# Optimization experiments

Hardware: AMD Instinct MI355X
Metric: run time of the kernel (lower is better)

The kernel has to match this reference:

```python
import jax, jax.numpy as jnp
import numpy as np

D_MODEL = 256      # num_nodes == d_model (forced by pre_relation mask shape)
MW = 2             # moving_window (hardcoded '2' in MPNN reshape)
STRIDE = 1
DECAY = 0.7
INPUT_DIM = 64
OUTPUT_DIM = 64
BN_EPS = 1e-5


def _mask_matrix():
    # Mask_Matrix: block (i,j) of size d_model x d_model equals decay**|i-j|
    blocks = DECAY ** np.abs(np.arange(MW)[:, None] - np.arange(MW)[None, :])
    return jnp.asarray(np.kron(blocks, np.ones((D_MODEL, D_MODEL))).astype(np.float32))


def _bn(h, w, b):
    # training-mode BatchNorm1d over channel-last layout [B, N, C]
    mu = h.mean(axis=(0, 1))
    var = h.var(axis=(0, 1))  # biased variance, as torch uses for normalization
    return (h - mu) * jax.lax.rsqrt(var + BN_EPS) * w + b


def setup_inputs() -> dict:
    key = jax.random.key(0)
    ks = jax.random.split(key, 4)
    bs, scale_num = 16, 17
    x = jax.random.normal(ks[0], (bs, scale_num, D_MODEL, INPUT_DIM), jnp.float32)
    # mapping2 weights scaled small to keep the dot-product softmax well conditioned
    w_map2 = jax.random.normal(ks[1], (INPUT_DIM, INPUT_DIM), jnp.float32) * 0.05
    b_map2 = jnp.zeros((INPUT_DIM,), jnp.float32)
    bn0_w = jnp.ones((INPUT_DIM,), jnp.float32)
    bn0_b = jnp.zeros((INPUT_DIM,), jnp.float32)
    th0_w = jax.random.normal(ks[2], (OUTPUT_DIM, INPUT_DIM), jnp.float32) / np.float32(np.sqrt(INPUT_DIM))
    th0_b = jnp.zeros((OUTPUT_DIM,), jnp.float32)
    th1_w = jax.random.normal(ks[3], (OUTPUT_DIM, INPUT_DIM), jnp.float32) / np.float32(np.sqrt(INPUT_DIM))
    th1_b = jnp.zeros((OUTPUT_DIM,), jnp.float32)
    bn1_w = jnp.ones((OUTPUT_DIM,), jnp.float32)
    bn1_b = jnp.zeros((OUTPUT_DIM,), jnp.float32)
    return dict(x=x, w_map2=w_map2, b_map2=b_map2, bn0_w=bn0_w, bn0_b=bn0_b,
                th0_w=th0_w, th0_b=th0_b, th1_w=th1_w, th1_b=th1_b,
                bn1_w=bn1_w, bn1_b=bn1_b)


def reference(x, w_map2, b_map2, bn0_w, bn0_b, th0_w, th0_b, th1_w, th1_b, bn1_w, bn1_b):
    bs, S, N, F = x.shape
    L = (S - MW) // STRIDE + 1  # num_windows from F.unfold
    # WindowConv_Graph + transpose(2,3) + reshape: X[b,l,m,n,f] = x[b, l*stride+m, n, f]
    idx = np.arange(L)[:, None] * STRIDE + np.arange(MW)[None, :]
    X = x[:, idx].reshape(bs * L, MW * N, F)  # [B', N1, F]

    # Dot_Graph_Construction_weights (N1 != d_model -> mapping2 branch)
    nf = X @ w_map2.T + b_map2                       # [B', N1, F]
    adj = jnp.einsum('bnf,bmf->bnm', nf, nf)         # [B', N1, N1]
    eye = jnp.eye(MW * N, dtype=x.dtype)
    adj = jax.nn.leaky_relu(adj - eye * 1e8)
    adj = jax.nn.softmax(adj, axis=-1) + eye

    # decay mask multiply
    adj = adj * _mask_matrix()

    # BatchNorm over input_dim channels
    xb = _bn(nf, bn0_w, bn0_b)

    # MPNN_mk_v2, field=2, way='sum'
    out = (adj @ xb) @ th0_w.T + th0_b               # hop 1
    adj2 = adj @ adj
    out = out + (adj2 @ xb) @ th1_w.T + th1_b        # hop 2
    out = jax.nn.leaky_relu(_bn(out, bn1_w, bn1_b))

    # pooling over the moving_window axis (mean), then over windows (mean)
    out = out.reshape(bs, L, MW, N, OUTPUT_DIM).mean(axis=2)
    return out.mean(axis=1)  # [bs, num_nodes, output_dim]
```

## Files before the change

kernel.cpp:

```cpp
#include <hip/hip_runtime.h>


typedef unsigned short u16;
typedef __bf16 bf16x8 __attribute__((ext_vector_type(8)));
typedef float f32x4 __attribute__((ext_vector_type(4)));
typedef unsigned int u32x4 __attribute__((ext_vector_type(4)));

#define MFMA16(a, b, c) __builtin_amdgcn_mfma_f32_16x16x32_bf16(a, b, c, 0, 0, 0)

#define BSZ 16
#define SNUM 17
#define FD 64
#define NB 256
#define N1 512
#define SL_ELEMS 16384
#define Y_ELEMS (BSZ * SNUM * SL_ELEMS)

#define WM_O 0
#define BM_O 4096
#define B0W_O 4160
#define B0B_O 4224
#define T0W_O 4288
#define T0B_O 8384
#define T1W_O 8448
#define T1B_O 12544
#define B1W_O 12608
#define B1B_O 12672
#define P_TOT 12736

#define SLAB2_O 32768
#define RED_O 65536
#define SCR_O 65792
#define LDS_BYTES ((SCR_O + 16 * 640) * 2)

__device__ __forceinline__ float bf2f(u16 u) {
    union { unsigned int i; float f; } v;
    v.i = ((unsigned int)u) << 16;
    return v.f;
}
__device__ __forceinline__ u16 f2bu(float f) {
    __bf16 h = (__bf16)f;
    return __builtin_bit_cast(u16, h);
}
__device__ __forceinline__ u16 f2bf(float f) {
    unsigned int u = __builtin_bit_cast(unsigned int, f);
    unsigned int r = (u + 0x7fffu + ((u >> 16) & 1u)) >> 16;
    return (u16)r;
}
__device__ __forceinline__ bf16x8 ld8g(const u16* p) {
    return __builtin_bit_cast(bf16x8, *reinterpret_cast<const u32x4*>(p));
}

__global__ __launch_bounds__(256) void k_prep(
    const void* p0, const void* p1, const void* p2, const void* p3,
    const void* p4, const void* p5, const void* p6, const void* p7,
    const void* p8, const void* p9, int* __restrict__ flagOut,
    u16* __restrict__ pc, float* __restrict__ stats) {
    const int tid = threadIdx.x, lane = tid & 63;
    int z = 0, bc = 0;
    const unsigned int* w = (const unsigned int*)p0;
    for (int i = lane; i < 2048; i += 64) {
        const unsigned int v = w[i];
        z += ((v & 0xffffu) == 0u);
        bc += (v >> 14) & 1;
    }
#pragma unroll
    for (int o = 1; o < 64; o <<= 1) {
        z += __shfl_xor(z, o);
        bc += __shfl_xor(bc, o);
    }
    const int flag = (z > 1024 || bc > 256) ? 1 : 0;
    if (blockIdx.x == 0) {
        if (tid == 0) *flagOut = flag;
        if (tid < 256) stats[tid] = 0.f;
    }
    const int i = blockIdx.x * 256 + tid;
    if (i >= P_TOT) return;
    const void* src;
    int si;
    if (i < BM_O)        { src = p0; si = i; }
    else if (i < B0W_O)  { src = p1; si = i - BM_O; }
    else if (i < B0B_O)  { src = p2; si = i - B0W_O; }
    else if (i < T0W_O)  { src = p3; si = i - B0B_O; }
    else if (i < T0B_O)  { src = p4; si = i - T0W_O; }
    else if (i < T1W_O)  { src = p5; si = i - T0B_O; }
    else if (i < T1B_O)  { src = p6; si = i - T1W_O; }
    else if (i < B1W_O)  { src = p7; si = i - T1B_O; }
    else if (i < B1B_O)  { src = p8; si = i - B1W_O; }
    else                 { src = p9; si = i - B1B_O; }
    pc[i] = flag ? f2bf(((const float*)src)[si]) : ((const u16*)src)[si];
}

__global__ __launch_bounds__(256) void k_y(const void* __restrict__ xv,
                                           const int* __restrict__ flag,
                                           const u16* __restrict__ pc,
                                           u16* __restrict__ y,
                                           float* __restrict__ gstats) {
    const int slice = blockIdx.x;
    const int tid = threadIdx.x, wave = tid >> 6, lane = tid & 63;
    const int quad = lane >> 4, l16 = lane & 15;
    __shared__ float red[128];
    if (tid < 128) red[tid] = 0.f;
    const int isf32 = *flag;

    f32x4 acc[4][4];
#pragma unroll
    for (int i = 0; i < 4; i++)
#pragma unroll
        for (int j = 0; j < 4; j++) acc[i][j] = (f32x4){0.f, 0.f, 0.f, 0.f};

    bf16x8 bfr[4][2];
#pragma unroll
    for (int nt = 0; nt < 4; nt++)
#pragma unroll
        for (int kh = 0; kh < 2; kh++)
            bfr[nt][kh] = ld8g(pc + WM_O + (nt * 16 + l16) * 64 + kh * 32 + quad * 8);

    const float* xf = (const float*)xv + (size_t)slice * SL_ELEMS;
    const u16* xh = (const u16*)xv + (size_t)slice * SL_ELEMS;

#pragma unroll
    for (int mt = 0; mt < 4; mt++) {
        const int row = wave * 64 + mt * 16 + l16;
        bf16x8 a0, a1;
        if (isf32) {
            const float* r0 = xf + row * 64 + quad * 8;
            f32x4 v0 = *(const f32x4*)r0;
            f32x4 v1 = *(const f32x4*)(r0 + 4);
            f32x4 v2 = *(const f32x4*)(r0 + 32);
            f32x4 v3 = *(const f32x4*)(r0 + 36);
#pragma unroll
            for (int j = 0; j < 4; j++) {
                a0[j] = (__bf16)v0[j]; a0[4 + j] = (__bf16)v1[j];
                a1[j] = (__bf16)v2[j]; a1[4 + j] = (__bf16)v3[j];
            }
        } else {
            a0 = ld8g(xh + row * 64 + quad * 8);
            a1 = ld8g(xh + row * 64 + 32 + quad * 8);
        }
#pragma unroll
        for (int nt = 0; nt < 4; nt++)
            acc[mt][nt] = MFMA16(a1, bfr[nt][1], MFMA16(a0, bfr[nt][0], acc[mt][nt]));
    }

    u16* ys = y + (size_t)slice * SL_ELEMS;
    float s1[4] = {0.f, 0.f, 0.f, 0.f}, s2[4] = {0.f, 0.f, 0.f, 0.f};
#pragma unroll
    for (int nt = 0; nt < 4; nt++) {
        const int col = nt * 16 + l16;
        const float bias = bf2f(pc[BM_O + col]);
#pragma unroll
        for (int mt = 0; mt < 4; mt++)
#pragma unroll
            for (int r = 0; r < 4; r++) {
                const int row = wave * 64 + mt * 16 + quad * 4 + r;
                const float v = acc[mt][nt][r] + bias;
                ys[row * 64 + col] = f2bu(v);
                s1[nt] += v;
                s2[nt] += v * v;
            }
        s1[nt] += __shfl_xor(s1[nt], 16); s1[nt] += __shfl_xor(s1[nt], 32);
        s2[nt] += __shfl_xor(s2[nt], 16); s2[nt] += __shfl_xor(s2[nt], 32);
    }
    __syncthreads();
    if (quad == 0) {
#pragma unroll
        for (int nt = 0; nt < 4; nt++) {
            atomicAdd(&red[nt * 16 + l16], s1[nt]);
            atomicAdd(&red[64 + nt * 16 + l16], s2[nt]);
        }
    }
    __syncthreads();
    const int s = slice % SNUM;
    const float wgt = (s == 0 || s == SNUM - 1) ? 1.f : 2.f;
    if (tid < 128) atomicAdd(&gstats[tid], red[tid] * wgt);
}

__global__ __launch_bounds__(1024)
__attribute__((amdgpu_waves_per_eu(4, 4)))
void k_mega(
    const u16* __restrict__ y, float* __restrict__ stats,
    const u16* __restrict__ pc, u16* __restrict__ opre) {
    extern __shared__ u16 lds[];
    u16* slab1 = lds;
    u16* slab2 = lds + SLAB2_O;
    float* red = (float*)(lds + RED_O);
    const int tid = threadIdx.x, w = tid >> 6, lane = tid & 63;
    const int quad = lane >> 4, l16 = lane & 15;
    u16* scr = lds + SCR_O + w * 640;
    const int p = blockIdx.x, b = p >> 4, l = p & 15;
    const f32x4 ZERO4 = (f32x4){0.f, 0.f, 0.f, 0.f};

    if (tid < 128) red[tid] = 0.f;

    const float cinv = 1.f / 131072.f;
    const int fme = tid & 63;
    float mu0 = stats[fme] * cinv;
    float vr0 = fmaxf(stats[64 + fme] * cinv - mu0 * mu0, 0.f);
    const float scale_f = rsqrtf(vr0 + 1e-5f) * bf2f(pc[B0W_O + fme]);
    const float shift_f = bf2f(pc[B0B_O + fme]) - mu0 * scale_f;

    const u16* ybase = y + (size_t)(b * SNUM + l) * SL_ELEMS;
#pragma unroll
    for (int i = 0; i < 4; i++) {
        const int gid = i * 1024 + tid, n = gid >> 3, g = gid & 7;
        *(u32x4*)(slab1 + n * 64 + ((g ^ (n & 7)) << 3)) =
            *(const u32x4*)(ybase + n * 64 + g * 8);
    }
    __syncthreads();

#pragma unroll
    for (int i = 0; i < 4; i++) {
        const int gn = (tid >> 6) + i * 16;
        union { u16 u[8]; u32x4 v; } pk;
#pragma unroll
        for (int j = 0; j < 8; j++) {
            const int n = gn * 8 + j;
            const u16 raw = slab1[n * 64 + (((fme >> 3) ^ (n & 7)) << 3) + (fme & 7)];
            pk.u[j] = f2bu(bf2f(raw) * scale_f + shift_f);
        }
        *(u32x4*)(slab2 + fme * 512 + ((gn ^ fme) << 3)) = pk.v;
    }
    __syncthreads();

    bf16x8 a[2][2];
#pragma unroll
    for (int st = 0; st < 2; st++)
#pragma unroll
        for (int h = 0; h < 2; h++) {
            const int row = w * 32 + st * 16 + l16;
            a[st][h] = *(const bf16x8*)(slab1 + row * 64 + (((h * 4 + quad) ^ (row & 7)) << 3));
        }

    for (int pass = 0; pass < 2; pass++) {
        f32x4 oacc[2][4];
        f32x4 lsum[2];
#pragma unroll
        for (int st = 0; st < 2; st++) {
            lsum[st] = ZERO4;
#pragma unroll
            for (int ft = 0; ft < 4; ft++) oacc[st][ft] = ZERO4;
        }

        for (int c = 0; c < 8; c++) {
            const float mf = ((w >= 8) == (c >= 4)) ? 1.f : 0.7f;
#pragma unroll
            for (int ch = 0; ch < 2; ch++) {
                const int colbase = c * 64 + ch * 32;
                f32x4 S[2][2];
#pragma unroll
                for (int jt = 0; jt < 2; jt++) {
                    const int rj = colbase + jt * 16 + l16;
                    const bf16x8 b0 = *(const bf16x8*)(slab1 + rj * 64 + ((quad ^ (rj & 7)) << 3));
                    const bf16x8 b1 = *(const bf16x8*)(slab1 + rj * 64 + (((4 + quad) ^ (rj & 7)) << 3));
#pragma unroll
                    for (int st = 0; st < 2; st++)
                        S[st][jt] = MFMA16(a[st][1], b1, MFMA16(a[st][0], b0, ZERO4));
                }
                bf16x8 pa[2];
#pragma unroll
                for (int st = 0; st < 2; st++) {
                    const int rowbase = w * 32 + st * 16;
#pragma unroll
                    for (int jt = 0; jt < 2; jt++)
#pragma unroll
                        for (int r = 0; r < 4; r++) {
                            const float s = S[st][jt][r];
                            const float m2 = s > 0.f ? 1.44269504f : 0.0144269504f;
                            float pv = exp2f(fminf(s * m2, 86.f));
                            if (colbase + jt * 16 == rowbase && l16 == quad * 4 + r) pv = 0.f;
                            lsum[st][r] += pv;
                            scr[(quad * 4 + r) * 40 + jt * 16 + l16] = f2bu(pv * mf);
                        }
                    pa[st] = *(const bf16x8*)(scr + l16 * 40 + quad * 8);
                }
#pragma unroll
                for (int ft = 0; ft < 4; ft++) {
                    const int f = ft * 16 + l16, gn = c * 8 + ch * 4 + quad;
                    const bf16x8 bv = *(const bf16x8*)(slab2 + f * 512 + ((gn ^ f) << 3));
                    oacc[0][ft] = MFMA16(pa[0], bv, oacc[0][ft]);
                    oacc[1][ft] = MFMA16(pa[1], bv, oacc[1][ft]);
                }
            }
        }
#pragma unroll
        for (int st = 0; st < 2; st++)
#pragma unroll
            for (int r = 0; r < 4; r++) {
                lsum[st][r] += __shfl_xor(lsum[st][r], 1);
                lsum[st][r] += __shfl_xor(lsum[st][r], 2);
                lsum[st][r] += __shfl_xor(lsum[st][r], 4);
                lsum[st][r] += __shfl_xor(lsum[st][r], 8);
            }

        if (pass == 0) {
#pragma unroll
            for (int st = 0; st < 2; st++) {
                f32x4 inv;
#pragma unroll
                for (int r = 0; r < 4; r++) inv[r] = __builtin_amdgcn_rcpf(lsum[st][r]);
#pragma unroll
                for (int ft = 0; ft < 4; ft++)
#pragma unroll
                    for (int r = 0; r < 4; r++) {
                        const int i = w * 32 + st * 16 + quad * 4 + r;
                        const int f = ft * 16 + l16;
                        const float xbv = bf2f(slab2[f * 512 + (((i >> 3) ^ f) << 3) + (i & 7)]);
                        oacc[st][ft][r] = oacc[st][ft][r] * inv[r] + xbv;
                    }
            }
            __syncthreads();
#pragma unroll
            for (int st = 0; st < 2; st++)
#pragma unroll
                for (int ft = 0; ft < 4; ft++)
#pragma unroll
                    for (int r = 0; r < 4; r++) {
                        const int i = w * 32 + st * 16 + quad * 4 + r;
                        const int f = ft * 16 + l16;
                        slab2[f * 512 + (((i >> 3) ^ f) << 3) + (i & 7)] = f2bu(oacc[st][ft][r]);
                    }
            __syncthreads();
        } else {
            float s1a[4] = {0.f, 0.f, 0.f, 0.f}, s2a[4] = {0.f, 0.f, 0.f, 0.f};
#pragma unroll
            for (int st = 0; st < 2; st++) {
                f32x4 inv;
#pragma unroll
                for (int r = 0; r < 4; r++) inv[r] = __builtin_amdgcn_rcpf(lsum[st][r]);
#pragma unroll
                for (int ft = 0; ft < 4; ft++)
#pragma unroll
                    for (int r = 0; r < 4; r++) {
                        const int i = w * 32 + st * 16 + quad * 4 + r;
                        const int f = ft * 16 + l16;
                        const float o1 = bf2f(slab2[f * 512 + (((i >> 3) ^ f) << 3) + (i & 7)]);
                        oacc[st][ft][r] = oacc[st][ft][r] * inv[r] + o1;
                    }
                bf16x8 a1[2], a2[2];
                const int irow = w * 32 + st * 16 + l16;
#pragma unroll
                for (int h = 0; h < 2; h++)
#pragma unroll
                    for (int j = 0; j < 8; j++) {
                        const int f = h * 32 + quad * 8 + j;
                        const u16 raw = slab2[f * 512 + (((irow >> 3) ^ f) << 3) + (irow & 7)];
                        a1[h][j] = __builtin_bit_cast(__bf16, raw);
                    }
#pragma unroll
                for (int h = 0; h < 2; h++) {
#pragma unroll
                    for (int ftl = 0; ftl < 2; ftl++)
#pragma unroll
                        for (int r = 0; r < 4; r++)
                            scr[(quad * 4 + r) * 40 + ftl * 16 + l16] = f2bu(oacc[st][2 * h + ftl][r]);
                    a2[h] = *(const bf16x8*)(scr + l16 * 40 + quad * 8);
                }
                f32x4 pacc[4];
#pragma unroll
                for (int ot = 0; ot < 4; ot++) {
                    const int o = ot * 16 + l16;
                    const float bias = bf2f(pc[T0B_O + o]) + bf2f(pc[T1B_O + o]);
                    pacc[ot] = (f32x4){bias, bias, bias, bias};
                }
#pragma unroll
                for (int h = 0; h < 2; h++)
#pragma unroll
                    for (int ot = 0; ot < 4; ot++) {
                        const int o = ot * 16 + l16;
                        bf16x8 w0f = ld8g(pc + T0W_O + o * 64 + h * 32 + quad * 8);
                        bf16x8 w1f = ld8g(pc + T1W_O + o * 64 + h * 32 + quad * 8);
                        pacc[ot] = MFMA16(a1[h], w0f, pacc[ot]);
                        pacc[ot] = MFMA16(a2[h], w1f, pacc[ot]);
                    }
#pragma unroll
                for (int ot = 0; ot < 4; ot++)
#pragma unroll
                    for (int r = 0; r < 4; r++) {
                        const int i = w * 32 + st * 16 + quad * 4 + r;
                        const int o = ot * 16 + l16;
                        const float v = pacc[ot][r];
                        s1a[ot] += v;
                        s2a[ot] += v * v;
                        opre[(size_t)p * (N1 * FD) + (size_t)i * 64 + o] = f2bu(v);
                    }
            }
#pragma unroll
            for (int ot = 0; ot < 4; ot++) {
                s1a[ot] += __shfl_xor(s1a[ot], 16); s1a[ot] += __shfl_xor(s1a[ot], 32);
                s2a[ot] += __shfl_xor(s2a[ot], 16); s2a[ot] += __shfl_xor(s2a[ot], 32);
            }
            if (quad == 0) {
#pragma unroll
                for (int ot = 0; ot < 4; ot++) {
                    atomicAdd(&red[ot * 16 + l16], s1a[ot]);
                    atomicAdd(&red[64 + ot * 16 + l16], s2a[ot]);
                }
            }
            __syncthreads();
            if (tid < 128) atomicAdd(&stats[128 + tid], red[tid]);
        }
    }
}

__global__ __launch_bounds__(256) void k_final(const u16* __restrict__ op,
                                               const float* __restrict__ stats,
                                               const u16* __restrict__ pc,
                                               float* __restrict__ out) {
    const int o = blockIdx.x * 256 + threadIdx.x;
    const int f = o & 63, n = (o >> 6) & 255, b = o >> 14;
    const float inv = 1.f / 131072.f;
    const float mu = stats[128 + f] * inv;
    const float var = fmaxf(stats[192 + f] * inv - mu * mu, 0.f);
    const float rs = rsqrtf(var + 1e-5f);
    const float scale = rs * bf2f(pc[B1W_O + f]);
    const float shift = bf2f(pc[B1B_O + f]) - mu * scale;
    float acc = 0.f;
    for (int l = 0; l < 16; l++) {
        const size_t pb = (size_t)(b * 16 + l) * N1 * FD;
#pragma unroll
        for (int m = 0; m < 2; m++) {
            float v = bf2f(op[pb + (size_t)(m * 256 + n) * 64 + f]);
            v = v * scale + shift;
            acc += (v > 0.f ? v : 0.01f * v);
        }
    }
    out[o] = acc * (1.f / 32.f);
}

extern "C" void kernel_launch(void* const* d_in, const int* in_sizes, int n_in,
                              void* d_out, int out_size, void* d_ws, size_t ws_size,
                              hipStream_t stream) {
    char* ws = (char*)d_ws;
    size_t off = 0;
    auto alloc = [&](size_t bytes) { void* pp = ws + off; off += (bytes + 255) & ~(size_t)255; return pp; };
    u16* y = (u16*)alloc((size_t)Y_ELEMS * 2);
    u16* opre = (u16*)alloc((size_t)NB * N1 * FD * 2);
    u16* pc = (u16*)alloc(P_TOT * 2);
    float* stats = (float*)alloc(256 * 4);
    int* flag = (int*)alloc(256);
    float* out = (float*)d_out;

    k_prep<<<50, 256, 0, stream>>>(d_in[1], d_in[2], d_in[3], d_in[4], d_in[5],
                                   d_in[6], d_in[7], d_in[8], d_in[9], d_in[10],
                                   flag, pc, stats);
    k_y<<<BSZ * SNUM, 256, 0, stream>>>(d_in[0], flag, pc, y, stats);
    k_mega<<<NB, 1024, LDS_BYTES, stream>>>(y, stats, pc, opre);
    k_final<<<1024, 256, 0, stream>>>(opre, stats, pc, out);
}
```

Baseline: 196.9 us.

## Split projection epilogue into separate kernel and fold decay mask into exponent

```diff
diff --git a/kernel.cpp b/kernel.cpp
--- a/kernel.cpp
+++ b/kernel.cpp
@@ -29,9 +29,8 @@
 #define P_TOT 12736
 
 #define SLAB2_O 32768
-#define RED_O 65536
-#define SCR_O 65792
-#define LDS_BYTES ((SCR_O + 16 * 640) * 2)
+#define SCR_O 65536
+#define LDS_U16 (SCR_O + 16 * 640)
 
 __device__ __forceinline__ float bf2f(u16 u) {
     union { unsigned int i; float f; } v;
@@ -179,19 +178,17 @@
 __global__ __launch_bounds__(1024)
 __attribute__((amdgpu_waves_per_eu(4, 4)))
 void k_mega(
-    const u16* __restrict__ y, float* __restrict__ stats,
-    const u16* __restrict__ pc, u16* __restrict__ opre) {
-    extern __shared__ u16 lds[];
+    const u16* __restrict__ y, const float* __restrict__ stats,
+    const u16* __restrict__ pc, u16* __restrict__ z1g,
+    float* __restrict__ pz1g) {
+    __shared__ u16 lds[LDS_U16];
     u16* slab1 = lds;
     u16* slab2 = lds + SLAB2_O;
-    float* red = (float*)(lds + RED_O);
     const int tid = threadIdx.x, w = tid >> 6, lane = tid & 63;
     const int quad = lane >> 4, l16 = lane & 15;
     u16* scr = lds + SCR_O + w * 640;
     const int p = blockIdx.x, b = p >> 4, l = p & 15;
     const f32x4 ZERO4 = (f32x4){0.f, 0.f, 0.f, 0.f};
-
-    if (tid < 128) red[tid] = 0.f;
 
     const float cinv = 1.f / 131072.f;
     const int fme = tid & 63;
@@ -232,6 +229,9 @@
             a[st][h] = *(const bf16x8*)(slab1 + row * 64 + (((h * 4 + quad) ^ (row & 7)) << 3));
         }
 
+    const float mb = (w < 8) ? 0.7f : (1.0f / 0.7f);
+    const float me = (w < 8) ? (1.0f / 0.7f) : 1.0f;
+
     for (int pass = 0; pass < 2; pass++) {
         f32x4 oacc[2][4];
         f32x4 lsum[2];
@@ -243,7 +243,13 @@
         }
 
         for (int c = 0; c < 8; c++) {
-            const float mf = ((w >= 8) == (c >= 4)) ? 1.f : 0.7f;
+            if (c == 4) {
+#pragma unroll
+                for (int st = 0; st < 2; st++)
+#pragma unroll
+                    for (int r = 0; r < 4; r++) lsum[st][r] *= mb;
+            }
+            const float lmf = ((w >= 8) == (c >= 4)) ? 0.f : -0.5145731728f;
 #pragma unroll
             for (int ch = 0; ch < 2; ch++) {
                 const int colbase = c * 64 + ch * 32;
@@ -267,10 +273,10 @@
                         for (int r = 0; r < 4; r++) {
                             const float s = S[st][jt][r];
                             const float m2 = s > 0.f ? 1.44269504f : 0.0144269504f;
-                            float pv = exp2f(fminf(s * m2, 86.f));
+                            float pv = exp2f(fminf(fmaf(s, m2, lmf), 86.f));
                             if (colbase + jt * 16 == rowbase && l16 == quad * 4 + r) pv = 0.f;
                             lsum[st][r] += pv;
-                            scr[(quad * 4 + r) * 40 + jt * 16 + l16] = f2bu(pv * mf);
+                            scr[(quad * 4 + r) * 40 + jt * 16 + l16] = f2bu(pv);
                         }
                     pa[st] = *(const bf16x8*)(scr + l16 * 40 + quad * 8);
                 }
@@ -298,7 +304,7 @@
             for (int st = 0; st < 2; st++) {
                 f32x4 inv;
 #pragma unroll
-                for (int r = 0; r < 4; r++) inv[r] = __builtin_amdgcn_rcpf(lsum[st][r]);
+                for (int r = 0; r < 4; r++) inv[r] = __builtin_amdgcn_rcpf(lsum[st][r] * me);
 #pragma unroll
                 for (int ft = 0; ft < 4; ft++)
 #pragma unroll
@@ -318,89 +324,104 @@
                     for (int r = 0; r < 4; r++) {
                         const int i = w * 32 + st * 16 + quad * 4 + r;
                         const int f = ft * 16 + l16;
-                        slab2[f * 512 + (((i >> 3) ^ f) << 3) + (i & 7)] = f2bu(oacc[st][ft][r]);
+                        const u16 hv = f2bu(oacc[st][ft][r]);
+                        slab2[f * 512 + (((i >> 3) ^ f) << 3) + (i & 7)] = hv;
+                        z1g[(size_t)p * (N1 * FD) + (size_t)i * 64 + f] = hv;
                     }
             __syncthreads();
         } else {
-            float s1a[4] = {0.f, 0.f, 0.f, 0.f}, s2a[4] = {0.f, 0.f, 0.f, 0.f};
 #pragma unroll
             for (int st = 0; st < 2; st++) {
                 f32x4 inv;
 #pragma unroll
-                for (int r = 0; r < 4; r++) inv[r] = __builtin_amdgcn_rcpf(lsum[st][r]);
+                for (int r = 0; r < 4; r++) inv[r] = __builtin_amdgcn_rcpf(lsum[st][r] * me);
 #pragma unroll
                 for (int ft = 0; ft < 4; ft++)
 #pragma unroll
                     for (int r = 0; r < 4; r++) {
                         const int i = w * 32 + st * 16 + quad * 4 + r;
                         const int f = ft * 16 + l16;
-                        const float o1 = bf2f(slab2[f * 512 + (((i >> 3) ^ f) << 3) + (i & 7)]);
-                        oacc[st][ft][r] = oacc[st][ft][r] * inv[r] + o1;
+                        pz1g[(size_t)p * (N1 * FD) + (size_t)i * 64 + f] =
+                            oacc[st][ft][r] * inv[r];
                     }
-                bf16x8 a1[2], a2[2];
-                const int irow = w * 32 + st * 16 + l16;
-#pragma unroll
-                for (int h = 0; h < 2; h++)
-#pragma unroll
-                    for (int j = 0; j < 8; j++) {
-                        const int f = h * 32 + quad * 8 + j;
-                        const u16 raw = slab2[f * 512 + (((irow >> 3) ^ f) << 3) + (irow & 7)];
-                        a1[h][j] = __builtin_bit_cast(__bf16, raw);
-                    }
-#pragma unroll
-                for (int h = 0; h < 2; h++) {
-#pragma unroll
-                    for (int ftl = 0; ftl < 2; ftl++)
-#pragma unroll
-                        for (int r = 0; r < 4; r++)
-                            scr[(quad * 4 + r) * 40 + ftl * 16 + l16] = f2bu(oacc[st][2 * h + ftl][r]);
-                    a2[h] = *(const bf16x8*)(scr + l16 * 40 + quad * 8);
-                }
-                f32x4 pacc[4];
-#pragma unroll
-                for (int ot = 0; ot < 4; ot++) {
-                    const int o = ot * 16 + l16;
-                    const float bias = bf2f(pc[T0B_O + o]) + bf2f(pc[T1B_O + o]);
-                    pacc[ot] = (f32x4){bias, bias, bias, bias};
-                }
-#pragma unroll
-                for (int h = 0; h < 2; h++)
-#pragma unroll
-                    for (int ot = 0; ot < 4; ot++) {
-                        const int o = ot * 16 + l16;
-                        bf16x8 w0f = ld8g(pc + T0W_O + o * 64 + h * 32 + quad * 8);
-                        bf16x8 w1f = ld8g(pc + T1W_O + o * 64 + h * 32 + quad * 8);
-                        pacc[ot] = MFMA16(a1[h], w0f, pacc[ot]);
-                        pacc[ot] = MFMA16(a2[h], w1f, pacc[ot]);
-                    }
-#pragma unroll
-                for (int ot = 0; ot < 4; ot++)
-#pragma unroll
-                    for (int r = 0; r < 4; r++) {
-                        const int i = w * 32 + st * 16 + quad * 4 + r;
-                        const int o = ot * 16 + l16;
-                        const float v = pacc[ot][r];
-                        s1a[ot] += v;
-                        s2a[ot] += v * v;
-                        opre[(size_t)p * (N1 * FD) + (size_t)i * 64 + o] = f2bu(v);
-                    }
-            }
+            }
+        }
+    }
+}
+
+__global__ __launch_bounds__(256) void k_proj(const u16* __restrict__ z1g,
+                                              const float* __restrict__ pz1g,
+                                              const u16* __restrict__ pc,
+                                              u16* __restrict__ opre,
+                                              float* __restrict__ gstats) {
+    const int g = blockIdx.x;
+    const int p = g >> 1, half = g & 1;
+    const int tid = threadIdx.x, wave = tid >> 6, lane = tid & 63;
+    const int quad = lane >> 4, l16 = lane & 15;
+    __shared__ float red[128];
+    if (tid < 128) red[tid] = 0.f;
+    const size_t base = (size_t)p * (N1 * FD);
+    float s1[4] = {0.f, 0.f, 0.f, 0.f}, s2[4] = {0.f, 0.f, 0.f, 0.f};
+#pragma unroll
+    for (int mt = 0; mt < 4; mt++) {
+        const int row = half * 256 + wave * 64 + mt * 16 + l16;
+        bf16x8 a1[2], a2[2];
+#pragma unroll
+        for (int h = 0; h < 2; h++) {
+            a1[h] = ld8g(z1g + base + row * 64 + h * 32 + quad * 8);
+            const float* pp = pz1g + base + row * 64 + h * 32 + quad * 8;
+            f32x4 q0 = *(const f32x4*)pp;
+            f32x4 q1 = *(const f32x4*)(pp + 4);
+#pragma unroll
+            for (int j = 0; j < 4; j++) {
+                a2[h][j] = (__bf16)(q0[j] + (float)a1[h][j]);
+                a2[h][4 + j] = (__bf16)(q1[j] + (float)a1[h][4 + j]);
+            }
+        }
+        f32x4 pacc[4];
+#pragma unroll
+        for (int ot = 0; ot < 4; ot++) {
+            const int o = ot * 16 + l16;
+            const float bias = bf2f(pc[T0B_O + o]) + bf2f(pc[T1B_O + o]);
+            pacc[ot] = (f32x4){bias, bias, bias, bias};
+        }
+#pragma unroll
+        for (int h = 0; h < 2; h++)
 #pragma unroll
             for (int ot = 0; ot < 4; ot++) {
-                s1a[ot] += __shfl_xor(s1a[ot], 16); s1a[ot] += __shfl_xor(s1a[ot], 32);
-                s2a[ot] += __shfl_xor(s2a[ot], 16); s2a[ot] += __shfl_xor(s2a[ot], 32);
-            }
-            if (quad == 0) {
-#pragma unroll
-                for (int ot = 0; ot < 4; ot++) {
-                    atomicAdd(&red[ot * 16 + l16], s1a[ot]);
-                    atomicAdd(&red[64 + ot * 16 + l16], s2a[ot]);
-                }
-            }
-            __syncthreads();
-            if (tid < 128) atomicAdd(&stats[128 + tid], red[tid]);
-        }
-    }
+                const int o = ot * 16 + l16;
+                bf16x8 w0f = ld8g(pc + T0W_O + o * 64 + h * 32 + quad * 8);
+                bf16x8 w1f = ld8g(pc + T1W_O + o * 64 + h * 32 + quad * 8);
+                pacc[ot] = MFMA16(a1[h], w0f, pacc[ot]);
+                pacc[ot] = MFMA16(a2[h], w1f, pacc[ot]);
+            }
+#pragma unroll
+        for (int ot = 0; ot < 4; ot++)
+#pragma unroll
+            for (int r = 0; r < 4; r++) {
+                const int i = half * 256 + wave * 64 + mt * 16 + quad * 4 + r;
+                const int o = ot * 16 + l16;
+                const float v = pacc[ot][r];
+                s1[ot] += v;
+                s2[ot] += v * v;
+                opre[base + (size_t)i * 64 + o] = f2bu(v);
+            }
+    }
+#pragma unroll
+    for (int ot = 0; ot < 4; ot++) {
+        s1[ot] += __shfl_xor(s1[ot], 16); s1[ot] += __shfl_xor(s1[ot], 32);
+        s2[ot] += __shfl_xor(s2[ot], 16); s2[ot] += __shfl_xor(s2[ot], 32);
+    }
+    __syncthreads();
+    if (quad == 0) {
+#pragma unroll
+        for (int ot = 0; ot < 4; ot++) {
+            atomicAdd(&red[ot * 16 + l16], s1[ot]);
+            atomicAdd(&red[64 + ot * 16 + l16], s2[ot]);
+        }
+    }
+    __syncthreads();
+    if (tid < 128) atomicAdd(&gstats[128 + tid], red[tid]);
 }
 
 __global__ __launch_bounds__(256) void k_final(const u16* __restrict__ op,
@@ -435,6 +456,8 @@
     size_t off = 0;
     auto alloc = [&](size_t bytes) { void* pp = ws + off; off += (bytes + 255) & ~(size_t)255; return pp; };
     u16* y = (u16*)alloc((size_t)Y_ELEMS * 2);
+    u16* z1 = (u16*)alloc((size_t)NB * N1 * FD * 2);
+    float* pz1 = (float*)alloc((size_t)NB * N1 * FD * 4);
     u16* opre = (u16*)alloc((size_t)NB * N1 * FD * 2);
     u16* pc = (u16*)alloc(P_TOT * 2);
     float* stats = (float*)alloc(256 * 4);
@@ -445,6 +468,7 @@
                                    d_in[6], d_in[7], d_in[8], d_in[9], d_in[10],
                                    flag, pc, stats);
     k_y<<<BSZ * SNUM, 256, 0, stream>>>(d_in[0], flag, pc, y, stats);
-    k_mega<<<NB, 1024, LDS_BYTES, stream>>>(y, stats, pc, opre);
+    k_mega<<<NB, 1024, 0, stream>>>(y, stats, pc, z1, pz1);
+    k_proj<<<512, 256, 0, stream>>>(z1, pz1, pc, opre, stats);
     k_final<<<1024, 256, 0, stream>>>(opre, stats, pc, out);
 }
```

Measured after the change: 225.7 us. +14.6%, slower.
